# Kernel optimization log

Hardware: AMD Instinct MI355X
Metric: run time of the kernel (lower is better)

## Reference

```python
import jax, jax.numpy as jnp
import numpy as np

NUM_JOINTS = 24
V = 6890
# standard SMPL kinematic tree (parent of joint i); index 0 is the root
PARENTS = [-1, 0, 0, 0, 1, 2, 3, 4, 5, 6, 7, 8, 9, 9, 9, 12, 13, 14, 16, 17, 18, 19, 20, 21]


def rodrigues(r):
    """Axis-angle [.., 3] -> rotation matrices [.., 3, 3] (batched Rodrigues)."""
    angle = jnp.sqrt(jnp.sum(r * r, axis=-1, keepdims=True) + 1e-16)
    axis = r / angle
    c = jnp.cos(angle)[..., None]
    s = jnp.sin(angle)[..., None]
    x, y, z = axis[..., 0], axis[..., 1], axis[..., 2]
    zeros = jnp.zeros_like(x)
    K = jnp.stack([zeros, -z, y, z, zeros, -x, -y, x, zeros], axis=-1).reshape(r.shape[:-1] + (3, 3))
    outer = axis[..., :, None] * axis[..., None, :]
    eye = jnp.eye(3, dtype=r.dtype)
    return c * eye + (1.0 - c) * outer + s * K


def with_zeros(Rt):
    """[B,3,4] -> [B,4,4] homogeneous transform."""
    B = Rt.shape[0]
    bottom = jnp.broadcast_to(jnp.array([0.0, 0.0, 0.0, 1.0], Rt.dtype), (B, 1, 4))
    return jnp.concatenate([Rt, bottom], axis=1)


def setup_inputs() -> dict:
    key = jax.random.key(0)
    ks = jax.random.split(key, 8)
    B = 1024
    return {
        "pose": jax.random.normal(ks[0], (B, 72), jnp.float32) * 0.3,
        "betas": jax.random.normal(ks[1], (B, 10), jnp.float32),
        "trans": jax.random.normal(ks[2], (B, 3), jnp.float32),
        "v_template": jax.random.normal(ks[3], (V, 3), jnp.float32),
        "shapedirs": jax.random.normal(ks[4], (V, 3, 10), jnp.float32) * 0.01,
        "posedirs": jax.random.normal(ks[5], (V, 3, 207), jnp.float32) * 0.01,
        "J_regressor": jax.random.uniform(ks[6], (24, V), jnp.float32) / V,
        "weights": jax.random.uniform(ks[7], (V, 24), jnp.float32),
    }


def reference(pose, betas, trans, v_template, shapedirs, posedirs, J_regressor, weights):
    B = pose.shape[0]
    dt = pose.dtype
    # pose -> per-joint rotation matrices [B,24,3,3]
    rot = rodrigues(pose.reshape(B, NUM_JOINTS, 3))
    root_rot = rot[:, 0]
    # pose blendshape features: non-root rotations minus identity, flattened [B,207]
    pose_map = (rot[:, 1:] - jnp.eye(3, dtype=dt)).reshape(B, (NUM_JOINTS - 1) * 9)
    v_shaped = v_template[None] + jnp.einsum('vcs,bs->bvc', shapedirs, betas)   # [B,V,3]
    j = jnp.einsum('jv,bvc->bjc', J_regressor, v_shaped)                        # [B,24,3]
    naked = v_shaped + jnp.einsum('vcp,bp->bvc', posedirs, pose_map)            # [B,V,3]
    v_posed = naked  # th_offsets is None
    # forward kinematics along the fixed 24-joint tree
    results = [None] * NUM_JOINTS
    results[0] = with_zeros(jnp.concatenate([root_rot, j[:, 0, :, None]], axis=2))
    for i in range(1, NUM_JOINTS):
        p = PARENTS[i]
        rel = with_zeros(jnp.concatenate([rot[:, i], (j[:, i] - j[:, p])[:, :, None]], axis=2))
        results[i] = results[p] @ rel
    G = jnp.stack(results, axis=1)  # [B,24,4,4] global transforms
    # remove rest-pose joint locations: G_rel = G - pack(G @ [j;0])
    j_h = jnp.concatenate([j, jnp.zeros((B, NUM_JOINTS, 1), dt)], axis=-1)      # [B,24,4]
    tmp = jnp.einsum('bjpq,bjq->bjp', G, j_h)                                   # [B,24,4]
    G_rel = G - jnp.concatenate([jnp.zeros(G.shape[:-1] + (3,), dt), tmp[..., None]], axis=-1)
    # linear blend skinning
    T = jnp.einsum('bjpq,vj->bpqv', G_rel, weights)                              # [B,4,4,V]
    rest_h = jnp.concatenate(
        [v_posed.transpose(0, 2, 1), jnp.ones((B, 1, v_posed.shape[1]), dt)], axis=1)  # [B,4,V]
    verts = jnp.einsum('bpqv,bqv->bvp', T, rest_h)[:, :, :3]                     # [B,V,3]
    jtr = G[:, :, :3, 3]                                                         # [B,24,3]
    # scale=1.0, normalise=False
    verts = verts + trans[:, None]
    jtr = jtr + trans[:, None]
    return verts, jtr, v_posed, naked, G
```

## Files before the change

kernel.cpp:

```cpp
#include <hip/hip_runtime.h>
#include <math.h>

#define V_NUM 6890
#define NJ 24
#define KTOT 217
#define KP 256
#define M_DIM (V_NUM * 3)
#define MPAD 20736
#define VPAD 6912

typedef __attribute__((ext_vector_type(8))) short bf16x8;
typedef __attribute__((ext_vector_type(4))) float f32x4;

__constant__ int c_parents[NJ] = {-1,0,0,0,1,2,3,4,5,6,7,8,9,9,9,12,13,14,16,17,18,19,20,21};

__device__ __forceinline__ unsigned short f2bf(float x) {
  union { float f; unsigned int u; } v; v.f = x;
  unsigned int r = v.u + 0x7fffu + ((v.u >> 16) & 1u);
  return (unsigned short)(r >> 16);
}

#define GLOBAL_AS __attribute__((address_space(1)))
#define LDS_AS __attribute__((address_space(3)))
__device__ __forceinline__ void gl_lds16(const void* g, void* l) {
  __builtin_amdgcn_global_load_lds((const GLOBAL_AS unsigned int*)g,
                                   (LDS_AS unsigned int*)l, 16, 0, 0);
}

__global__ __launch_bounds__(256) void k_regress2(
    const float* __restrict__ JR, const float* __restrict__ SD,
    const float* __restrict__ VT, float* __restrict__ JS, float* __restrict__ Jt) {
  int j = blockIdx.x;
  int q = blockIdx.y;
  int tid = threadIdx.x;
  float part = 0.f;
  const float* jr = JR + (size_t)j * V_NUM;
  if (q < 30) {
    for (int v = tid; v < V_NUM; v += 256)
      part += jr[v] * SD[(size_t)v * 30 + q];
  } else {
    int cc = q - 30;
    for (int v = tid; v < V_NUM; v += 256)
      part += jr[v] * VT[(size_t)v * 3 + cc];
  }
  for (int off = 32; off > 0; off >>= 1) part += __shfl_down(part, off);
  __shared__ float sm[4];
  if ((tid & 63) == 0) sm[tid >> 6] = part;
  __syncthreads();
  if (tid == 0) {
    float s = sm[0] + sm[1] + sm[2] + sm[3];
    if (q < 30) JS[j * 30 + q] = s;
    else Jt[j * 3 + (q - 30)] = s;
  }
}

__global__ __launch_bounds__(256) void k_conv(
    const float* __restrict__ SD, const float* __restrict__ PD,
    const float* __restrict__ W,
    unsigned short* __restrict__ Abf, unsigned short* __restrict__ Wbf) {
  int bid = blockIdx.x;
  int tid = threadIdx.x;
  if (bid < MPAD) {
    int m = bid, k = tid;
    float v = 0.f;
    if (m < M_DIM && k < KTOT)
      v = (k < 10) ? SD[(size_t)m * 10 + k] : PD[(size_t)m * 207 + (k - 10)];
    Abf[(size_t)m * KP + k] = f2bf(v);
  } else {
    int idx = (bid - MPAD) * 256 + tid;
    if (idx < VPAD * 32) {
      int v = idx >> 5, k = idx & 31;
      Wbf[idx] = (v < V_NUM && k < NJ) ? f2bf(W[(size_t)v * NJ + k]) : (unsigned short)0;
    }
  }
}

__global__ __launch_bounds__(64) void k_batch(
    const float* __restrict__ pose, const float* __restrict__ betas,
    const float* __restrict__ trans, const float* __restrict__ JS,
    const float* __restrict__ Jt, unsigned short* __restrict__ Kcb,
    unsigned short* __restrict__ GrelP, float* __restrict__ outG,
    float* __restrict__ outJtr, int B) {
  int b = blockIdx.x;
  int lane = threadIdx.x;
  __shared__ float rotS[NJ][9];
  __shared__ float jS[NJ * 3];
  __shared__ float Gs[NJ][12];
  __shared__ float GrS[NJ][12];

  if (lane < NJ) {
    float rx = pose[b * 72 + lane * 3 + 0];
    float ry = pose[b * 72 + lane * 3 + 1];
    float rz = pose[b * 72 + lane * 3 + 2];
    float a2 = rx * rx + ry * ry + rz * rz + 1e-16f;
    float ang = sqrtf(a2);
    float inv = 1.f / ang;
    float ux = rx * inv, uy = ry * inv, uz = rz * inv;
    float c = cosf(ang), s = sinf(ang), ic = 1.f - c;
    float R[9];
    R[0] = c + ic * ux * ux;      R[1] = ic * ux * uy - s * uz; R[2] = ic * ux * uz + s * uy;
    R[3] = ic * uy * ux + s * uz; R[4] = c + ic * uy * uy;      R[5] = ic * uy * uz - s * ux;
    R[6] = ic * uz * ux - s * uy; R[7] = ic * uz * uy + s * ux; R[8] = c + ic * uz * uz;
#pragma unroll
    for (int k = 0; k < 9; k++) rotS[lane][k] = R[k];
    if (lane > 0) {
#pragma unroll
      for (int k = 0; k < 9; k++) {
        float iden = (k == 0 || k == 4 || k == 8) ? 1.f : 0.f;
        Kcb[(size_t)b * KP + 10 + (lane - 1) * 9 + k] = f2bf(R[k] - iden);
      }
    }
  }
  if (lane < 10) Kcb[(size_t)b * KP + lane] = f2bf(betas[b * 10 + lane]);
  if (lane < KP - KTOT) Kcb[(size_t)b * KP + KTOT + lane] = 0;

  __syncthreads();
  for (int idx = lane; idx < 72; idx += 64) {
    float s = Jt[idx];
#pragma unroll
    for (int ss = 0; ss < 10; ss++) s += JS[idx * 10 + ss] * betas[b * 10 + ss];
    jS[idx] = s;
  }
  __syncthreads();

  if (lane == 0) {
#pragma unroll
    for (int p = 0; p < 3; p++) {
      Gs[0][p * 4 + 0] = rotS[0][p * 3 + 0];
      Gs[0][p * 4 + 1] = rotS[0][p * 3 + 1];
      Gs[0][p * 4 + 2] = rotS[0][p * 3 + 2];
      Gs[0][p * 4 + 3] = jS[p];
    }
    for (int i = 1; i < NJ; i++) {
      int par = c_parents[i];
      float t0 = jS[i * 3 + 0] - jS[par * 3 + 0];
      float t1 = jS[i * 3 + 1] - jS[par * 3 + 1];
      float t2 = jS[i * 3 + 2] - jS[par * 3 + 2];
#pragma unroll
      for (int p = 0; p < 3; p++) {
        float rp0 = Gs[par][p * 4 + 0], rp1 = Gs[par][p * 4 + 1], rp2 = Gs[par][p * 4 + 2];
#pragma unroll
        for (int q = 0; q < 3; q++) {
          Gs[i][p * 4 + q] = rp0 * rotS[i][0 * 3 + q] + rp1 * rotS[i][1 * 3 + q] + rp2 * rotS[i][2 * 3 + q];
        }
        Gs[i][p * 4 + 3] = rp0 * t0 + rp1 * t1 + rp2 * t2 + Gs[par][p * 4 + 3];
      }
    }
    for (int i = 0; i < NJ; i++) {
      float jx = jS[i * 3 + 0], jy = jS[i * 3 + 1], jz = jS[i * 3 + 2];
#pragma unroll
      for (int p = 0; p < 3; p++) {
        float g0 = Gs[i][p * 4 + 0], g1 = Gs[i][p * 4 + 1], g2 = Gs[i][p * 4 + 2];
        GrS[i][p * 4 + 0] = g0;
        GrS[i][p * 4 + 1] = g1;
        GrS[i][p * 4 + 2] = g2;
        GrS[i][p * 4 + 3] = Gs[i][p * 4 + 3] - (g0 * jx + g1 * jy + g2 * jz);
      }
    }
  }
  __syncthreads();

  for (int idx = lane; idx < NJ * 16; idx += 64) {
    int jj = idx >> 4, rc = idx & 15, p = rc >> 2, q = rc & 3;
    float val = (p < 3) ? Gs[jj][p * 4 + q] : ((q == 3) ? 1.f : 0.f);
    outG[(size_t)b * NJ * 16 + idx] = val;
  }
  for (int idx = lane; idx < NJ * 3; idx += 64) {
    int jj = idx / 3, p = idx % 3;
    outJtr[(size_t)b * NJ * 3 + idx] = Gs[jj][p * 4 + 3] + trans[b * 3 + p];
  }
  for (int idx = lane; idx < 16 * 40; idx += 64) {
    int c = idx / 40, j = idx % 40;
    GrelP[(size_t)b * 640 + idx] = (c < 12 && j < NJ) ? f2bf(GrS[j][c]) : (unsigned short)0;
  }
}

__global__ __launch_bounds__(256) void k_pose_mfma(
    const unsigned short* __restrict__ Kcb, const unsigned short* __restrict__ Abf,
    const float* __restrict__ VT, float* __restrict__ outVP, int B) {
  __shared__ char ldsraw[65536];

  const int tid = threadIdx.x;
  const int lane = tid & 63;
  const int w = tid >> 6;
  const int wr = w >> 1, wc = w & 1;
  const int b0 = blockIdx.y * 128;
  const int m0 = blockIdx.x * 128;

  f32x4 vt4[4];
  {
    int mbase = m0 + wr * 64 + ((lane >> 4) << 4);
#pragma unroll
    for (int i = 0; i < 4; i++) {
      int mm = mbase + i * 4;
      if (mm + 3 < M_DIM) vt4[i] = *(const f32x4*)(VT + mm);
      else {
#pragma unroll
        for (int r = 0; r < 4; r++) vt4[i][r] = (mm + r < M_DIM) ? VT[mm + r] : 0.f;
      }
    }
  }

  f32x4 acc[4][4];
#pragma unroll
  for (int i = 0; i < 4; i++)
#pragma unroll
    for (int j = 0; j < 4; j++) acc[i][j] = (f32x4){0.f, 0.f, 0.f, 0.f};

  int Lrow[4], Lkb[4];
#pragma unroll
  for (int i = 0; i < 4; i++) {
    int L = w * 4096 + i * 1024 + lane * 16;
    int row = L >> 7;
    int kb = (L & 127) ^ ((row & 7) << 4);
    Lrow[i] = row;
    Lkb[i] = kb >> 1;
  }

#define STAGE(kt, c)                                                              \
  {                                                                               \
    char* bufA = ldsraw + (c) * 32768;                                            \
    char* bufB = bufA + 16384;                                                    \
    _Pragma("unroll")                                                             \
    for (int i = 0; i < 4; i++) {                                                 \
      const unsigned short* gA = Kcb + (size_t)(b0 + Lrow[i]) * KP + (kt) * 64 + Lkb[i]; \
      gl_lds16(gA, bufA + w * 4096 + i * 1024);                                   \
      const unsigned short* gB = Abf + (size_t)(m0 + Lrow[i]) * KP + (kt) * 64 + Lkb[i]; \
      gl_lds16(gB, bufB + w * 4096 + i * 1024);                                   \
    }                                                                             \
  }

  STAGE(0, 0);
  __syncthreads();

#pragma unroll
  for (int kt = 0; kt < 4; ++kt) {
    int cur = kt & 1;
    if (kt < 3) STAGE(kt + 1, cur ^ 1);
    const char* At = ldsraw + cur * 32768;
    const char* Bt = At + 16384;
#pragma unroll
    for (int h = 0; h < 2; ++h) {
      bf16x8 fm[4], fb[4];
#pragma unroll
      for (int fi = 0; fi < 4; fi++) {
        int row = wr * 64 + fi * 16 + (lane & 15);
        int byte = (row << 7) + ((h * 64 + ((lane >> 4) << 4)) ^ ((row & 7) << 4));
        fm[fi] = *(const bf16x8*)(Bt + byte);
      }
#pragma unroll
      for (int fj = 0; fj < 4; fj++) {
        int row = wc * 64 + fj * 16 + (lane & 15);
        int byte = (row << 7) + ((h * 64 + ((lane >> 4) << 4)) ^ ((row & 7) << 4));
        fb[fj] = *(const bf16x8*)(At + byte);
      }
#pragma unroll
      for (int fi = 0; fi < 4; fi++)
#pragma unroll
        for (int fj = 0; fj < 4; fj++)
          acc[fi][fj] = __builtin_amdgcn_mfma_f32_16x16x32_bf16(fm[fi], fb[fj], acc[fi][fj], 0, 0, 0);
    }
    __syncthreads();
  }
#undef STAGE

  char* wslab = ldsraw + w * 4352;
  const int a = lane & 15, c = lane >> 4;
  const int xr = (lane & 3) << 4;
#pragma unroll
  for (int fj = 0; fj < 4; fj++) {
#pragma unroll
    for (int fi = 0; fi < 4; fi++) {
      int off = a * 272 + (((fi << 6) + (c << 4)) ^ xr);
      *(f32x4*)(wslab + off) = acc[fi][fj];
    }
    int brow = b0 + wc * 64 + fj * 16 + a;
    size_t gb = (size_t)brow * M_DIM;
    int mg0 = m0 + wr * 64 + (c << 4);
#pragma unroll
    for (int i = 0; i < 4; i++) {
      int off = a * 272 + (((c << 6) + (i << 4)) ^ xr);
      f32x4 v = *(f32x4*)(wslab + off);
      v = v + vt4[i];
      int mg = mg0 + i * 4;
      if (mg + 3 < M_DIM) {
        *(f32x4*)(outVP + gb + mg) = v;
      } else {
#pragma unroll
        for (int r = 0; r < 4; r++)
          if (mg + r < M_DIM) outVP[gb + mg + r] = v[r];
      }
    }
  }
}

__global__ __launch_bounds__(256) void k_skin7(
    const float* __restrict__ VP, const unsigned short* __restrict__ Wbf,
    const unsigned short* __restrict__ GrelP, const float* __restrict__ trans,
    float* __restrict__ outNK, float* __restrict__ outVerts, int B) {
  __shared__ float Tl[4][64 * 13];
  const int tid = threadIdx.x;
  const int lane = tid & 63;
  const int w = tid >> 6;
  const int vl16 = lane & 15;
  const int p = lane >> 4;
  const int kb = p * 8;
  const int vbase = blockIdx.x * 256 + w * 64;
  const int b0 = blockIdx.y * 4;
  const int vg = vbase + lane;
  const bool vok = vg < V_NUM;

  bf16x8 wf[4];
#pragma unroll
  for (int sub = 0; sub < 4; sub++)
    wf[sub] = *(const bf16x8*)(Wbf + (size_t)(vbase + sub * 16 + vl16) * 32 + kb);

  bf16x8 af[4];
#pragma unroll
  for (int bi = 0; bi < 4; bi++)
    af[bi] = *(const bf16x8*)(GrelP + (size_t)(b0 + bi) * 640 + vl16 * 40 + kb);

  float* myT = Tl[w];

  float xc0 = 0.f, xc1 = 0.f, xc2 = 0.f;
  if (vok) {
    const float* xp = VP + (size_t)b0 * M_DIM + (size_t)vg * 3;
    xc0 = xp[0]; xc1 = xp[1]; xc2 = xp[2];
  }

#pragma unroll
  for (int bi = 0; bi < 4; bi++) {
    int b = b0 + bi;
    f32x4 acc[4];
#pragma unroll
    for (int sub = 0; sub < 4; sub++) {
      f32x4 z = (f32x4){0.f, 0.f, 0.f, 0.f};
      acc[sub] = __builtin_amdgcn_mfma_f32_16x16x32_bf16(af[bi], wf[sub], z, 0, 0, 0);
    }
    if (p < 3) {
#pragma unroll
      for (int sub = 0; sub < 4; sub++) {
        int vi = sub * 16 + vl16;
#pragma unroll
        for (int r = 0; r < 4; r++)
          myT[vi * 13 + p * 4 + r] = acc[sub][r];
      }
    }
    float xn0 = 0.f, xn1 = 0.f, xn2 = 0.f;
    if (bi < 3 && vok) {
      const float* xp = VP + (size_t)(b + 1) * M_DIM + (size_t)vg * 3;
      xn0 = xp[0]; xn1 = xp[1]; xn2 = xp[2];
    }
    if (vok) {
      size_t base = (size_t)b * M_DIM + (size_t)vg * 3;
      float* onk = outNK + base;
      onk[0] = xc0; onk[1] = xc1; onk[2] = xc2;
      float t[12];
#pragma unroll
      for (int c = 0; c < 12; c++) t[c] = myT[lane * 13 + c];
      float* op = outVerts + base;
      op[0] = t[0] * xc0 + t[1] * xc1 + t[2] * xc2 + t[3] + trans[b * 3 + 0];
      op[1] = t[4] * xc0 + t[5] * xc1 + t[6] * xc2 + t[7] + trans[b * 3 + 1];
      op[2] = t[8] * xc0 + t[9] * xc1 + t[10] * xc2 + t[11] + trans[b * 3 + 2];
    }
    xc0 = xn0; xc1 = xn1; xc2 = xn2;
  }
}

extern "C" void kernel_launch(void* const* d_in, const int* in_sizes, int n_in,
                              void* d_out, int out_size, void* d_ws, size_t ws_size,
                              hipStream_t stream) {
  const float* pose  = (const float*)d_in[0];
  const float* betas = (const float*)d_in[1];
  const float* trans = (const float*)d_in[2];
  const float* vt    = (const float*)d_in[3];
  const float* sd    = (const float*)d_in[4];
  const float* pd    = (const float*)d_in[5];
  const float* jreg  = (const float*)d_in[6];
  const float* wgt   = (const float*)d_in[7];
  int B = in_sizes[0] / 72;

  float* out = (float*)d_out;
  size_t nvb = (size_t)B * M_DIM;
  float* o_verts = out;
  float* o_jtr   = o_verts + nvb;
  float* o_vp    = o_jtr + (size_t)B * NJ * 3;
  float* o_nk    = o_vp + nvb;
  float* o_G     = o_nk + nvb;

  char* wsb = (char*)d_ws;
  float* JS = (float*)wsb;
  float* Jt = JS + 720;
  size_t off = (720 + 72) * 4;
  unsigned short* Kcb   = (unsigned short*)(wsb + off);
  unsigned short* Abf   = (unsigned short*)(wsb + off + (size_t)B * KP * 2);
  unsigned short* GrelP = Abf + (size_t)MPAD * KP;
  unsigned short* Wbf   = GrelP + (size_t)B * 640;

  dim3 gR(24, 33);
  k_regress2<<<gR, 256, 0, stream>>>(jreg, sd, vt, JS, Jt);
  k_conv<<<MPAD + (VPAD * 32 + 255) / 256, 256, 0, stream>>>(sd, pd, wgt, Abf, Wbf);
  k_batch<<<B, 64, 0, stream>>>(pose, betas, trans, JS, Jt, Kcb, GrelP, o_G, o_jtr, B);
  dim3 gC(MPAD / 128, B / 128);
  k_pose_mfma<<<gC, 256, 0, stream>>>(Kcb, Abf, vt, o_vp, B);
  dim3 gD(VPAD / 256, B / 4);
  k_skin7<<<gD, 256, 0, stream>>>(o_vp, Wbf, GrelP, trans, o_nk, o_verts, B);
}
```

Measured before the change: 147.5 us.

## Single-buffer pose GEMM LDS and use swizzled vector LDS transform in skinning

The pose-blendshape MFMA kernel drops its double-buffered LDS staging (64KB to 32KB). It now loads each K tile, syncs, then computes, which lets more blocks fit per CU but gives up overlap between loads and compute. The skinning kernel stores the per-vertex 4x4 transform rows into a 16-float padded LDS slab with an XOR swizzle. It writes and reads them as 128-bit vectors instead of 12 scalar accesses per lane, aiming to reduce LDS instruction count and bank conflicts.

```diff
diff --git a/kernel.cpp b/kernel.cpp
--- a/kernel.cpp
+++ b/kernel.cpp
@@ -178,7 +178,7 @@
 __global__ __launch_bounds__(256) void k_pose_mfma(
     const unsigned short* __restrict__ Kcb, const unsigned short* __restrict__ Abf,
     const float* __restrict__ VT, float* __restrict__ outVP, int B) {
-  __shared__ char ldsraw[65536];
+  __shared__ char ldsraw[32768];
 
   const int tid = threadIdx.x;
   const int lane = tid & 63;
@@ -217,28 +217,18 @@
     Lkb[i] = kb >> 1;
   }
 
-#define STAGE(kt, c)                                                              \
-  {                                                                               \
-    char* bufA = ldsraw + (c) * 32768;                                            \
-    char* bufB = bufA + 16384;                                                    \
-    _Pragma("unroll")                                                             \
-    for (int i = 0; i < 4; i++) {                                                 \
-      const unsigned short* gA = Kcb + (size_t)(b0 + Lrow[i]) * KP + (kt) * 64 + Lkb[i]; \
-      gl_lds16(gA, bufA + w * 4096 + i * 1024);                                   \
-      const unsigned short* gB = Abf + (size_t)(m0 + Lrow[i]) * KP + (kt) * 64 + Lkb[i]; \
-      gl_lds16(gB, bufB + w * 4096 + i * 1024);                                   \
-    }                                                                             \
-  }
-
-  STAGE(0, 0);
-  __syncthreads();
-
 #pragma unroll
   for (int kt = 0; kt < 4; ++kt) {
-    int cur = kt & 1;
-    if (kt < 3) STAGE(kt + 1, cur ^ 1);
-    const char* At = ldsraw + cur * 32768;
-    const char* Bt = At + 16384;
+    char* At = ldsraw;
+    char* Bt = ldsraw + 16384;
+#pragma unroll
+    for (int i = 0; i < 4; i++) {
+      const unsigned short* gA = Kcb + (size_t)(b0 + Lrow[i]) * KP + kt * 64 + Lkb[i];
+      gl_lds16(gA, At + w * 4096 + i * 1024);
+      const unsigned short* gB = Abf + (size_t)(m0 + Lrow[i]) * KP + kt * 64 + Lkb[i];
+      gl_lds16(gB, Bt + w * 4096 + i * 1024);
+    }
+    __syncthreads();
 #pragma unroll
     for (int h = 0; h < 2; ++h) {
       bf16x8 fm[4], fb[4];
@@ -262,7 +252,6 @@
     }
     __syncthreads();
   }
-#undef STAGE
 
   char* wslab = ldsraw + w * 4352;
   const int a = lane & 15, c = lane >> 4;
@@ -294,11 +283,11 @@
   }
 }
 
-__global__ __launch_bounds__(256) void k_skin7(
+__global__ __launch_bounds__(256) void k_skin9(
     const float* __restrict__ VP, const unsigned short* __restrict__ Wbf,
     const unsigned short* __restrict__ GrelP, const float* __restrict__ trans,
     float* __restrict__ outNK, float* __restrict__ outVerts, int B) {
-  __shared__ float Tl[4][64 * 13];
+  __shared__ float Tl[4][64 * 16];
   const int tid = threadIdx.x;
   const int lane = tid & 63;
   const int w = tid >> 6;
@@ -309,6 +298,7 @@
   const int b0 = blockIdx.y * 4;
   const int vg = vbase + lane;
   const bool vok = vg < V_NUM;
+  const int kx = (lane >> 1) & 3;
 
   bf16x8 wf[4];
 #pragma unroll
@@ -337,14 +327,11 @@
       f32x4 z = (f32x4){0.f, 0.f, 0.f, 0.f};
       acc[sub] = __builtin_amdgcn_mfma_f32_16x16x32_bf16(af[bi], wf[sub], z, 0, 0, 0);
     }
-    if (p < 3) {
-#pragma unroll
-      for (int sub = 0; sub < 4; sub++) {
-        int vi = sub * 16 + vl16;
-#pragma unroll
-        for (int r = 0; r < 4; r++)
-          myT[vi * 13 + p * 4 + r] = acc[sub][r];
-      }
+#pragma unroll
+    for (int sub = 0; sub < 4; sub++) {
+      int vi = sub * 16 + vl16;
+      int slot = p ^ ((vi >> 1) & 3);
+      *(f32x4*)&myT[vi * 16 + slot * 4] = acc[sub];
     }
     float xn0 = 0.f, xn1 = 0.f, xn2 = 0.f;
     if (bi < 3 && vok) {
@@ -352,16 +339,16 @@
       xn0 = xp[0]; xn1 = xp[1]; xn2 = xp[2];
     }
     if (vok) {
+      f32x4 ta = *(f32x4*)&myT[lane * 16 + ((0 ^ kx) << 2)];
+      f32x4 tb = *(f32x4*)&myT[lane * 16 + ((1 ^ kx) << 2)];
+      f32x4 tc = *(f32x4*)&myT[lane * 16 + ((2 ^ kx) << 2)];
       size_t base = (size_t)b * M_DIM + (size_t)vg * 3;
       float* onk = outNK + base;
       onk[0] = xc0; onk[1] = xc1; onk[2] = xc2;
-      float t[12];
-#pragma unroll
-      for (int c = 0; c < 12; c++) t[c] = myT[lane * 13 + c];
       float* op = outVerts + base;
-      op[0] = t[0] * xc0 + t[1] * xc1 + t[2] * xc2 + t[3] + trans[b * 3 + 0];
-      op[1] = t[4] * xc0 + t[5] * xc1 + t[6] * xc2 + t[7] + trans[b * 3 + 1];
-      op[2] = t[8] * xc0 + t[9] * xc1 + t[10] * xc2 + t[11] + trans[b * 3 + 2];
+      op[0] = ta[0] * xc0 + ta[1] * xc1 + ta[2] * xc2 + ta[3] + trans[b * 3 + 0];
+      op[1] = tb[0] * xc0 + tb[1] * xc1 + tb[2] * xc2 + tb[3] + trans[b * 3 + 1];
+      op[2] = tc[0] * xc0 + tc[1] * xc1 + tc[2] * xc2 + tc[3] + trans[b * 3 + 2];
     }
     xc0 = xn0; xc1 = xn1; xc2 = xn2;
   }
@@ -404,5 +391,5 @@
   dim3 gC(MPAD / 128, B / 128);
   k_pose_mfma<<<gC, 256, 0, stream>>>(Kcb, Abf, vt, o_vp, B);
   dim3 gD(VPAD / 256, B / 4);
-  k_skin7<<<gD, 256, 0, stream>>>(o_vp, Wbf, GrelP, trans, o_nk, o_verts, B);
-}
+  k_skin9<<<gD, 256, 0, stream>>>(o_vp, Wbf, GrelP, trans, o_nk, o_verts, B);
+}
```

New measurement: 149.2 us. About the same (+1.2%).
